# Performance work log

Measured on AMD Instinct MI355X. Metric: run time of the kernel, lower is better.

Reference implementation:

```python
import jax, jax.numpy as jnp
import numpy as np

NUM_SEGMENTS = 64  # number of bags
L, D, F = 1024, 256, 32  # D = L/4, F = D/8, K = 1
EPS = 1e-12  # torch F.normalize eps


def setup_inputs() -> dict:
    key = jax.random.key(0)
    ks = jax.random.split(key, 10)
    N = 262144
    x = jax.random.normal(ks[0], (N, L), dtype=jnp.float32)
    idxs = jnp.sort(jax.random.randint(ks[1], (N,), 0, NUM_SEGMENTS)).astype(jnp.int64)
    sc = lambda fan_in: 1.0 / np.sqrt(fan_in)
    W1 = jax.random.uniform(ks[2], (L, D), jnp.float32, -sc(L), sc(L))
    b1 = jax.random.uniform(ks[3], (D,), jnp.float32, -sc(L), sc(L))
    Wa1 = jax.random.uniform(ks[4], (D, F), jnp.float32, -sc(D), sc(D))
    ba1 = jax.random.uniform(ks[5], (F,), jnp.float32, -sc(D), sc(D))
    Wa2 = jax.random.uniform(ks[6], (F, 1), jnp.float32, -sc(F), sc(F))
    ba2 = jax.random.uniform(ks[7], (1,), jnp.float32, -sc(F), sc(F))
    Wp = jax.random.uniform(ks[8], (D, F), jnp.float32, -sc(D), sc(D))
    bp = jax.random.uniform(ks[9], (F,), jnp.float32, -sc(D), sc(D))
    return {"x": x, "idxs": idxs, "W1": W1, "b1": b1, "Wa1": Wa1, "ba1": ba1,
            "Wa2": Wa2, "ba2": ba2, "Wp": Wp, "bp": bp}


def reference(x, idxs, W1, b1, Wa1, ba1, Wa2, ba2, Wp, bp):
    seg = idxs.astype(jnp.int32)
    # feature extractor (Dropout is identity in eval): H [N, D]
    H = x @ W1 + b1
    # attention logits: tanh MLP -> [N]
    logits = (jnp.tanh(H @ Wa1 + ba1) @ Wa2 + ba2)[:, 0]
    # segment softmax over instances within each bag
    m = jax.ops.segment_max(logits, seg, num_segments=NUM_SEGMENTS)
    e = jnp.exp(logits - m[seg])
    s = jax.ops.segment_sum(e, seg, num_segments=NUM_SEGMENTS)
    w = e / s[seg]  # [N]
    # attention-weighted bag embeddings: M [B, D]
    M = jax.ops.segment_sum(w[:, None] * H, seg, num_segments=NUM_SEGMENTS)
    # projector + L2 normalize (torch F.normalize: x / max(||x||, eps))
    proj = M @ Wp + bp
    norm = jnp.linalg.norm(proj, axis=1, keepdims=True)
    proj = proj / jnp.maximum(norm, EPS)
    return (M, proj)
```

## Files before the change

### kernel.cpp

```cpp
#include <hip/hip_runtime.h>
#include <stdint.h>

#define LDIM 1024
#define DDIM 256
#define FDIM 32
#define NSEG 64
#define BM 64
#define BK 64

typedef __attribute__((ext_vector_type(4))) float f32x4;
typedef __attribute__((ext_vector_type(8))) short short8;
typedef __attribute__((ext_vector_type(4))) unsigned int u32x4;

__device__ __forceinline__ unsigned int pk2bf(float a, float b) {
  union { float f; unsigned int u; } x, y; x.f = a; y.f = b;
  unsigned int ua = x.u + 0x7FFFu + ((x.u >> 16) & 1u);
  unsigned int ub = y.u + 0x7FFFu + ((y.u >> 16) & 1u);
  return (ua >> 16) | (ub & 0xFFFF0000u);
}

__device__ __forceinline__ unsigned short f2bf(float f) {
  union { float f; unsigned int u; } v; v.f = f;
  unsigned int r = v.u + 0x7FFFu + ((v.u >> 16) & 1u);
  return (unsigned short)(r >> 16);
}

__device__ __forceinline__ short8 pack8(f32x4 a, f32x4 b) {
  union { u32x4 u; short8 s; } r;
  r.u[0] = pk2bf(a[0], a[1]); r.u[1] = pk2bf(a[2], a[3]);
  r.u[2] = pk2bf(b[0], b[1]); r.u[3] = pk2bf(b[2], b[3]);
  return r.s;
}

__global__ void prep_w1t(const float* __restrict__ W1, const float* __restrict__ Wa1,
                         unsigned short* __restrict__ w1t) {
  __shared__ float rowf[DDIM];
  const int k = blockIdx.x;
  const int t = threadIdx.x;
  float v = W1[(size_t)k * DDIM + t];
  rowf[t] = v;
  w1t[(size_t)t * LDIM + k] = f2bf(v);
  __syncthreads();
  if (t < FDIM) {
    float a = 0.f;
    for (int c = 0; c < DDIM; ++c) a += rowf[c] * Wa1[c * FDIM + t];
    w1t[(size_t)(DDIM + t) * LDIM + k] = f2bf(a);
  }
}

__global__ void prep_misc(const float* __restrict__ b1, const float* __restrict__ Wa1,
                          const float* __restrict__ ba1, float* __restrict__ bz,
                          float* __restrict__ acc_eh, float* __restrict__ accE) {
  const int b = blockIdx.x, t = threadIdx.x;
  acc_eh[b * DDIM + t] = 0.f;
  if (t == 0) accE[b] = 0.f;
  if (b == 0 && t < FDIM) {
    float a = ba1[t];
    for (int c = 0; c < DDIM; ++c) a += b1[c] * Wa1[c * FDIM + t];
    bz[t] = a;
  }
}

__global__ __launch_bounds__(256, 3) void fused_main(
    const float* __restrict__ x, const int* __restrict__ idxs,
    const unsigned short* __restrict__ w1t, const float* __restrict__ bz,
    const float* __restrict__ Wa2, const float* __restrict__ ba2,
    float* __restrict__ acc_eh, float* __restrict__ accE)
{
  __shared__ __align__(16) unsigned char blds[288 * 128];
  __shared__ float logit_s[BM];
  __shared__ float e_s[BM];
  __shared__ int seg_s[BM];

  const int tid = threadIdx.x;
  const int lane = tid & 63;
  const int wid = tid >> 6;
  const int g = lane >> 4;
  const int cl = lane & 15;
  const int row0 = blockIdx.x * BM;

  if (tid < BM) seg_s[tid] = idxs[row0 + tid];

  f32x4 acc[18];
  const f32x4 zero4 = {0.f, 0.f, 0.f, 0.f};
  #pragma unroll
  for (int n = 0; n < 18; ++n) acc[n] = zero4;

  const char* w1tb = (const char*)w1t;
  const float* gxa = x + (size_t)(row0 + wid * 16 + cl) * LDIM + g * 8;

  f32x4 s0, s1, s2, s3;
  s0 = *(const f32x4*)(gxa);      s1 = *(const f32x4*)(gxa + 4);
  s2 = *(const f32x4*)(gxa + 32); s3 = *(const f32x4*)(gxa + 36);

  #pragma unroll 1
  for (int kt = 0; kt < 16; ++kt) {
    __builtin_amdgcn_s_barrier();
    #pragma unroll
    for (int j = 0; j < 9; ++j) {
      int byteoff = j * 4096 + tid * 16;
      int brow = byteoff >> 7;
      int bcolb = byteoff & 127;
      int srcb = brow * 2048 + kt * 128 + (bcolb ^ ((brow & 7) << 4));
      __builtin_amdgcn_global_load_lds(
          (const __attribute__((address_space(1))) unsigned int*)(w1tb + srcb),
          (__attribute__((address_space(3))) unsigned int*)(blds + j * 4096 + wid * 1024),
          16, 0, 0);
    }
    short8 af0 = pack8(s0, s1);
    short8 af1 = pack8(s2, s3);
    __syncthreads();
    if (kt < 15) {
      const float* gp = gxa + (kt + 1) * 64;
      s0 = *(const f32x4*)(gp);      s1 = *(const f32x4*)(gp + 4);
      s2 = *(const f32x4*)(gp + 32); s3 = *(const f32x4*)(gp + 36);
    }
    #pragma unroll
    for (int kk = 0; kk < 2; ++kk) {
      #pragma unroll
      for (int n = 0; n < 18; ++n) {
        int brr = n * 16 + cl;
        short8 bf = *(const short8*)(blds + brr * 128 + ((kk * 64 + g * 16) ^ ((cl & 7) << 4)));
        acc[n] = __builtin_amdgcn_mfma_f32_16x16x32_bf16(kk ? af1 : af0, bf, acc[n], 0, 0, 0);
      }
    }
  }

  {
    const float w2a = Wa2[cl], w2b = Wa2[16 + cl];
    const float bza = bz[cl], bzb = bz[16 + cl];
    float p[4];
    #pragma unroll
    for (int q = 0; q < 4; ++q) {
      float ea = exp2f((acc[16][q] + bza) * 2.8853900817779268f);
      float eb = exp2f((acc[17][q] + bzb) * 2.8853900817779268f);
      p[q] = (1.f - 2.f / (ea + 1.f)) * w2a + (1.f - 2.f / (eb + 1.f)) * w2b;
    }
    #pragma unroll
    for (int mask = 1; mask <= 8; mask <<= 1)
      #pragma unroll
      for (int q = 0; q < 4; ++q) p[q] += __shfl_xor(p[q], mask);
    if (cl == 0) {
      #pragma unroll
      for (int q = 0; q < 4; ++q)
        logit_s[wid * 16 + g * 4 + q] = p[q];
    }
  }
  __syncthreads();
  if (tid < BM) e_s[tid] = expf(logit_s[tid] + ba2[0]);
  __syncthreads();

  const int smin = seg_s[0];
  const int smax = seg_s[BM - 1];
  float ev[4]; int sv[4];
  #pragma unroll
  for (int q = 0; q < 4; ++q) {
    int rl = wid * 16 + g * 4 + q;
    ev[q] = e_s[rl];
    sv[q] = seg_s[rl];
  }
  for (int s = smin; s <= smax; ++s) {
    float wv[4];
    #pragma unroll
    for (int q = 0; q < 4; ++q) wv[q] = (sv[q] == s) ? ev[q] : 0.f;
    #pragma unroll
    for (int n = 0; n < 16; ++n) {
      float cs = 0.f;
      #pragma unroll
      for (int q = 0; q < 4; ++q) cs += wv[q] * acc[n][q];
      cs += __shfl_xor(cs, 16);
      cs += __shfl_xor(cs, 32);
      if (lane < 16) atomicAdd(&acc_eh[s * DDIM + n * 16 + cl], cs);
    }
    if (wid == 0) {
      float v = (seg_s[lane] == s) ? e_s[lane] : 0.f;
      #pragma unroll
      for (int mask = 1; mask <= 32; mask <<= 1) v += __shfl_xor(v, mask);
      if (lane == 0) atomicAdd(&accE[s], v);
    }
  }
}

__global__ void finalize_k(const float* __restrict__ acc_eh, const float* __restrict__ accE,
                           const float* __restrict__ b1, const float* __restrict__ Wp,
                           const float* __restrict__ bp, float* __restrict__ out) {
  __shared__ float Ml[DDIM];
  const int s = blockIdx.x, t = threadIdx.x;
  const float E = accE[s];
  float m = 0.f;
  if (E > 0.f) m = acc_eh[s * DDIM + t] / E + b1[t];
  out[s * DDIM + t] = m;
  Ml[t] = m;
  __syncthreads();
  if (t < FDIM) {
    float p = bp[t];
    for (int c = 0; c < DDIM; ++c) p += Ml[c] * Wp[c * FDIM + t];
    float n2 = p * p;
    #pragma unroll
    for (int mask = 1; mask <= 16; mask <<= 1) n2 += __shfl_xor(n2, mask);
    out[NSEG * DDIM + s * FDIM + t] = p / fmaxf(sqrtf(n2), 1e-12f);
  }
}

extern "C" void kernel_launch(void* const* d_in, const int* in_sizes, int n_in,
                              void* d_out, int out_size, void* d_ws, size_t ws_size,
                              hipStream_t stream) {
  const float* x   = (const float*)d_in[0];
  const int*   idxs= (const int*)d_in[1];
  const float* W1  = (const float*)d_in[2];
  const float* b1  = (const float*)d_in[3];
  const float* Wa1 = (const float*)d_in[4];
  const float* ba1 = (const float*)d_in[5];
  const float* Wa2 = (const float*)d_in[6];
  const float* ba2 = (const float*)d_in[7];
  const float* Wp  = (const float*)d_in[8];
  const float* bp  = (const float*)d_in[9];
  float* out = (float*)d_out;

  char* ws = (char*)d_ws;
  unsigned short* w1t = (unsigned short*)ws;
  float* bz     = (float*)(ws + 655360);
  float* acc_eh = (float*)(ws + 655488);
  float* accE   = (float*)(ws + 721024);

  const int n = in_sizes[1];
  prep_w1t<<<LDIM, DDIM, 0, stream>>>(W1, Wa1, w1t);
  prep_misc<<<NSEG, DDIM, 0, stream>>>(b1, Wa1, ba1, bz, acc_eh, accE);
  fused_main<<<n / BM, 256, 0, stream>>>(x, idxs, w1t, bz, Wa2, ba2, acc_eh, accE);
  finalize_k<<<NSEG, DDIM, 0, stream>>>(acc_eh, accE, b1, Wp, bp, out);
}
```

Before: 308.0 us.

## Pool raw inputs per segment and apply W1 after pooling

Uses linearity to skip computing H = x@W1 for every row. The main kernel now computes only the 32-wide attention projection z = x@(W1·Wa1) with MFMA. It accumulates exp-weighted raw x rows per segment (1024 wide) through global atomics, and the finalize kernel multiplies the pooled vector by W1. This removes most of the MFMA work, leaving the kernel bound by streaming x. The cost is many more global atomics per segment, since there are 1024 columns instead of 256, split-K partial sums reduced through LDS atomics, and a bf16-rounded x used for the weighted sum.

```diff
diff --git a/kernel.cpp b/kernel.cpp
--- a/kernel.cpp
+++ b/kernel.cpp
@@ -5,8 +5,7 @@
 #define DDIM 256
 #define FDIM 32
 #define NSEG 64
-#define BM 64
-#define BK 64
+#define BM 32
 
 typedef __attribute__((ext_vector_type(4))) float f32x4;
 typedef __attribute__((ext_vector_type(8))) short short8;
@@ -32,27 +31,33 @@
   return r.s;
 }
 
-__global__ void prep_w1t(const float* __restrict__ W1, const float* __restrict__ Wa1,
-                         unsigned short* __restrict__ w1t) {
+__device__ __forceinline__ float bflo(unsigned int u) {
+  union { unsigned int u; float f; } v; v.u = u << 16; return v.f;
+}
+__device__ __forceinline__ float bfhi(unsigned int u) {
+  union { unsigned int u; float f; } v; v.u = u & 0xFFFF0000u; return v.f;
+}
+
+__global__ void prep_w1tz(const float* __restrict__ W1, const float* __restrict__ Wa1,
+                          unsigned short* __restrict__ w1tz) {
   __shared__ float rowf[DDIM];
   const int k = blockIdx.x;
   const int t = threadIdx.x;
-  float v = W1[(size_t)k * DDIM + t];
-  rowf[t] = v;
-  w1t[(size_t)t * LDIM + k] = f2bf(v);
+  rowf[t] = W1[(size_t)k * DDIM + t];
   __syncthreads();
   if (t < FDIM) {
     float a = 0.f;
     for (int c = 0; c < DDIM; ++c) a += rowf[c] * Wa1[c * FDIM + t];
-    w1t[(size_t)(DDIM + t) * LDIM + k] = f2bf(a);
+    w1tz[(size_t)t * LDIM + k] = f2bf(a);
   }
 }
 
 __global__ void prep_misc(const float* __restrict__ b1, const float* __restrict__ Wa1,
                           const float* __restrict__ ba1, float* __restrict__ bz,
-                          float* __restrict__ acc_eh, float* __restrict__ accE) {
+                          float* __restrict__ Xacc, float* __restrict__ accE) {
   const int b = blockIdx.x, t = threadIdx.x;
-  acc_eh[b * DDIM + t] = 0.f;
+  #pragma unroll
+  for (int i = 0; i < 4; ++i) Xacc[b * LDIM + i * DDIM + t] = 0.f;
   if (t == 0) accE[b] = 0.f;
   if (b == 0 && t < FDIM) {
     float a = ba1[t];
@@ -63,132 +68,148 @@
 
 __global__ __launch_bounds__(256, 3) void fused_main(
     const float* __restrict__ x, const int* __restrict__ idxs,
-    const unsigned short* __restrict__ w1t, const float* __restrict__ bz,
+    const unsigned short* __restrict__ w1tz, const float* __restrict__ bz,
     const float* __restrict__ Wa2, const float* __restrict__ ba2,
-    float* __restrict__ acc_eh, float* __restrict__ accE)
+    float* __restrict__ Xacc, float* __restrict__ accE)
 {
-  __shared__ __align__(16) unsigned char blds[288 * 128];
-  __shared__ float logit_s[BM];
-  __shared__ float e_s[BM];
-  __shared__ int seg_s[BM];
+  __shared__ float zlds[BM][33];
+  __shared__ float e_lds[BM];
+  __shared__ int   seg_lds[BM];
 
   const int tid = threadIdx.x;
   const int lane = tid & 63;
-  const int wid = tid >> 6;
+  const int w = tid >> 6;
   const int g = lane >> 4;
   const int cl = lane & 15;
   const int row0 = blockIdx.x * BM;
-
-  if (tid < BM) seg_s[tid] = idxs[row0 + tid];
-
-  f32x4 acc[18];
-  const f32x4 zero4 = {0.f, 0.f, 0.f, 0.f};
-  #pragma unroll
-  for (int n = 0; n < 18; ++n) acc[n] = zero4;
-
-  const char* w1tb = (const char*)w1t;
-  const float* gxa = x + (size_t)(row0 + wid * 16 + cl) * LDIM + g * 8;
-
-  f32x4 s0, s1, s2, s3;
-  s0 = *(const f32x4*)(gxa);      s1 = *(const f32x4*)(gxa + 4);
-  s2 = *(const f32x4*)(gxa + 32); s3 = *(const f32x4*)(gxa + 36);
-
-  #pragma unroll 1
-  for (int kt = 0; kt < 16; ++kt) {
-    __builtin_amdgcn_s_barrier();
-    #pragma unroll
-    for (int j = 0; j < 9; ++j) {
-      int byteoff = j * 4096 + tid * 16;
-      int brow = byteoff >> 7;
-      int bcolb = byteoff & 127;
-      int srcb = brow * 2048 + kt * 128 + (bcolb ^ ((brow & 7) << 4));
-      __builtin_amdgcn_global_load_lds(
-          (const __attribute__((address_space(1))) unsigned int*)(w1tb + srcb),
-          (__attribute__((address_space(3))) unsigned int*)(blds + j * 4096 + wid * 1024),
-          16, 0, 0);
-    }
-    short8 af0 = pack8(s0, s1);
-    short8 af1 = pack8(s2, s3);
-    __syncthreads();
-    if (kt < 15) {
-      const float* gp = gxa + (kt + 1) * 64;
-      s0 = *(const f32x4*)(gp);      s1 = *(const f32x4*)(gp + 4);
-      s2 = *(const f32x4*)(gp + 32); s3 = *(const f32x4*)(gp + 36);
-    }
+  const int kw = w * 256;
+
+  for (int i = tid; i < BM * 33; i += 256) ((float*)zlds)[i] = 0.f;
+  if (tid < BM) seg_lds[tid] = idxs[row0 + tid];
+  __syncthreads();
+
+  const float* xa0 = x + (size_t)(row0 + cl) * LDIM + kw + g * 8;
+  const float* xa1 = xa0 + (size_t)16 * LDIM;
+  const unsigned short* wz = w1tz + kw + (size_t)g * 8;
+
+  f32x4 zacc[2][2];
+  #pragma unroll
+  for (int m = 0; m < 2; ++m)
+    #pragma unroll
+    for (int n = 0; n < 2; ++n) zacc[m][n] = (f32x4){0.f, 0.f, 0.f, 0.f};
+
+  short8 xf[4][2][2];
+
+  #pragma unroll
+  for (int ktl = 0; ktl < 4; ++ktl) {
     #pragma unroll
     for (int kk = 0; kk < 2; ++kk) {
-      #pragma unroll
-      for (int n = 0; n < 18; ++n) {
-        int brr = n * 16 + cl;
-        short8 bf = *(const short8*)(blds + brr * 128 + ((kk * 64 + g * 16) ^ ((cl & 7) << 4)));
-        acc[n] = __builtin_amdgcn_mfma_f32_16x16x32_bf16(kk ? af1 : af0, bf, acc[n], 0, 0, 0);
-      }
-    }
-  }
-
-  {
-    const float w2a = Wa2[cl], w2b = Wa2[16 + cl];
-    const float bza = bz[cl], bzb = bz[16 + cl];
-    float p[4];
-    #pragma unroll
-    for (int q = 0; q < 4; ++q) {
-      float ea = exp2f((acc[16][q] + bza) * 2.8853900817779268f);
-      float eb = exp2f((acc[17][q] + bzb) * 2.8853900817779268f);
-      p[q] = (1.f - 2.f / (ea + 1.f)) * w2a + (1.f - 2.f / (eb + 1.f)) * w2b;
-    }
+      {
+        const float* p = xa0 + ktl * 64 + kk * 32;
+        xf[ktl][0][kk] = pack8(*(const f32x4*)p, *(const f32x4*)(p + 4));
+      }
+      {
+        const float* p = xa1 + ktl * 64 + kk * 32;
+        xf[ktl][1][kk] = pack8(*(const f32x4*)p, *(const f32x4*)(p + 4));
+      }
+      #pragma unroll
+      for (int n = 0; n < 2; ++n) {
+        short8 bf = *(const short8*)(wz + (size_t)(n * 16 + cl) * LDIM + ktl * 64 + kk * 32);
+        zacc[0][n] = __builtin_amdgcn_mfma_f32_16x16x32_bf16(xf[ktl][0][kk], bf, zacc[0][n], 0, 0, 0);
+        zacc[1][n] = __builtin_amdgcn_mfma_f32_16x16x32_bf16(xf[ktl][1][kk], bf, zacc[1][n], 0, 0, 0);
+      }
+    }
+    __builtin_amdgcn_sched_barrier(0);
+  }
+
+  #pragma unroll
+  for (int m = 0; m < 2; ++m)
+    #pragma unroll
+    for (int n = 0; n < 2; ++n)
+      #pragma unroll
+      for (int q = 0; q < 4; ++q)
+        atomicAdd(&zlds[m * 16 + g * 4 + q][n * 16 + cl], zacc[m][n][q]);
+  __syncthreads();
+
+  if (tid < BM) {
+    const int r = tid;
+    float lg = 0.f;
+    #pragma unroll
+    for (int c = 0; c < 32; ++c) {
+      float e2 = exp2f((zlds[r][c] + bz[c]) * 2.8853900817779268f);
+      lg += (1.f - 2.f / (e2 + 1.f)) * Wa2[c];
+    }
+    e_lds[r] = expf(lg + ba2[0]);
+  }
+  __syncthreads();
+
+  const float ea = e_lds[cl];
+  const float eb = e_lds[16 + cl];
+  const int   sa = seg_lds[cl];
+  const int   sb = seg_lds[16 + cl];
+  const int smin = seg_lds[0];
+  const int smax = seg_lds[BM - 1];
+
+  for (int s = smin; s <= smax; ++s) {
+    const float wa = (sa == s) ? ea : 0.f;
+    const float wb = (sb == s) ? eb : 0.f;
+    float pt[4][2][8];
+    #pragma unroll
+    for (int ktl = 0; ktl < 4; ++ktl)
+      #pragma unroll
+      for (int kk = 0; kk < 2; ++kk) {
+        union { short8 s8; u32x4 u; } ua, ub;
+        ua.s8 = xf[ktl][0][kk];
+        ub.s8 = xf[ktl][1][kk];
+        #pragma unroll
+        for (int p2 = 0; p2 < 4; ++p2) {
+          pt[ktl][kk][p2 * 2]     = wa * bflo(ua.u[p2]) + wb * bflo(ub.u[p2]);
+          pt[ktl][kk][p2 * 2 + 1] = wa * bfhi(ua.u[p2]) + wb * bfhi(ub.u[p2]);
+        }
+      }
     #pragma unroll
     for (int mask = 1; mask <= 8; mask <<= 1)
       #pragma unroll
-      for (int q = 0; q < 4; ++q) p[q] += __shfl_xor(p[q], mask);
+      for (int ktl = 0; ktl < 4; ++ktl)
+        #pragma unroll
+        for (int kk = 0; kk < 2; ++kk)
+          #pragma unroll
+          for (int j = 0; j < 8; ++j)
+            pt[ktl][kk][j] += __shfl_xor(pt[ktl][kk][j], mask);
     if (cl == 0) {
-      #pragma unroll
-      for (int q = 0; q < 4; ++q)
-        logit_s[wid * 16 + g * 4 + q] = p[q];
-    }
-  }
-  __syncthreads();
-  if (tid < BM) e_s[tid] = expf(logit_s[tid] + ba2[0]);
-  __syncthreads();
-
-  const int smin = seg_s[0];
-  const int smax = seg_s[BM - 1];
-  float ev[4]; int sv[4];
-  #pragma unroll
-  for (int q = 0; q < 4; ++q) {
-    int rl = wid * 16 + g * 4 + q;
-    ev[q] = e_s[rl];
-    sv[q] = seg_s[rl];
-  }
-  for (int s = smin; s <= smax; ++s) {
-    float wv[4];
-    #pragma unroll
-    for (int q = 0; q < 4; ++q) wv[q] = (sv[q] == s) ? ev[q] : 0.f;
-    #pragma unroll
-    for (int n = 0; n < 16; ++n) {
-      float cs = 0.f;
-      #pragma unroll
-      for (int q = 0; q < 4; ++q) cs += wv[q] * acc[n][q];
-      cs += __shfl_xor(cs, 16);
-      cs += __shfl_xor(cs, 32);
-      if (lane < 16) atomicAdd(&acc_eh[s * DDIM + n * 16 + cl], cs);
-    }
-    if (wid == 0) {
-      float v = (seg_s[lane] == s) ? e_s[lane] : 0.f;
-      #pragma unroll
-      for (int mask = 1; mask <= 32; mask <<= 1) v += __shfl_xor(v, mask);
+      float* dst = Xacc + s * LDIM + kw + g * 8;
+      #pragma unroll
+      for (int ktl = 0; ktl < 4; ++ktl)
+        #pragma unroll
+        for (int kk = 0; kk < 2; ++kk)
+          #pragma unroll
+          for (int j = 0; j < 8; ++j)
+            atomicAdd(dst + ktl * 64 + kk * 32 + j, pt[ktl][kk][j]);
+    }
+    if (w == 0) {
+      float v = (lane < BM && seg_lds[lane & 31] == s) ? e_lds[lane & 31] : 0.f;
+      v += __shfl_xor(v, 1); v += __shfl_xor(v, 2); v += __shfl_xor(v, 4);
+      v += __shfl_xor(v, 8); v += __shfl_xor(v, 16);
       if (lane == 0) atomicAdd(&accE[s], v);
     }
   }
 }
 
-__global__ void finalize_k(const float* __restrict__ acc_eh, const float* __restrict__ accE,
-                           const float* __restrict__ b1, const float* __restrict__ Wp,
-                           const float* __restrict__ bp, float* __restrict__ out) {
+__global__ void finalize_k(const float* __restrict__ Xacc, const float* __restrict__ accE,
+                           const float* __restrict__ W1, const float* __restrict__ b1,
+                           const float* __restrict__ Wp, const float* __restrict__ bp,
+                           float* __restrict__ out) {
+  __shared__ float Xn[LDIM];
   __shared__ float Ml[DDIM];
   const int s = blockIdx.x, t = threadIdx.x;
   const float E = accE[s];
+  const float inv = (E > 0.f) ? 1.f / E : 0.f;
+  #pragma unroll
+  for (int i = 0; i < 4; ++i) Xn[i * DDIM + t] = Xacc[s * LDIM + i * DDIM + t] * inv;
+  __syncthreads();
   float m = 0.f;
-  if (E > 0.f) m = acc_eh[s * DDIM + t] / E + b1[t];
+  for (int k = 0; k < LDIM; ++k) m += Xn[k] * W1[(size_t)k * DDIM + t];
+  m = (E > 0.f) ? (m + b1[t]) : 0.f;
   out[s * DDIM + t] = m;
   Ml[t] = m;
   __syncthreads();
@@ -218,14 +239,14 @@
   float* out = (float*)d_out;
 
   char* ws = (char*)d_ws;
-  unsigned short* w1t = (unsigned short*)ws;
-  float* bz     = (float*)(ws + 655360);
-  float* acc_eh = (float*)(ws + 655488);
-  float* accE   = (float*)(ws + 721024);
+  unsigned short* w1tz = (unsigned short*)ws;
+  float* bz   = (float*)(ws + 65536);
+  float* Xacc = (float*)(ws + 65536 + 256);
+  float* accE = (float*)(ws + 65536 + 256 + 262144);
 
   const int n = in_sizes[1];
-  prep_w1t<<<LDIM, DDIM, 0, stream>>>(W1, Wa1, w1t);
-  prep_misc<<<NSEG, DDIM, 0, stream>>>(b1, Wa1, ba1, bz, acc_eh, accE);
-  fused_main<<<n / BM, 256, 0, stream>>>(x, idxs, w1t, bz, Wa2, ba2, acc_eh, accE);
-  finalize_k<<<NSEG, DDIM, 0, stream>>>(acc_eh, accE, b1, Wp, bp, out);
-}
+  prep_w1tz<<<LDIM, DDIM, 0, stream>>>(W1, Wa1, w1tz);
+  prep_misc<<<NSEG, DDIM, 0, stream>>>(b1, Wa1, ba1, bz, Xacc, accE);
+  fused_main<<<n / BM, 256, 0, stream>>>(x, idxs, w1tz, bz, Wa2, ba2, Xacc, accE);
+  finalize_k<<<NSEG, DDIM, 0, stream>>>(Xacc, accE, W1, b1, Wp, bp, out);
+}
```

New measurement: 938.8 us. +204.8%, slower.
